# Performance work log

Measured on AMD Instinct MI355X. Metric: run time of the kernel, lower is better.

The kernel has to match this reference:

```python
import jax, jax.numpy as jnp
import numpy as np

N_HEAD = 16
D_MODEL = 1024
D_HEAD = D_MODEL // N_HEAD
B, T = 2, 2048


def setup_inputs() -> dict:
    key = jax.random.key(0)
    k1, k2, k3 = jax.random.split(key, 3)
    x = jax.random.normal(k1, (B, T, D_MODEL), dtype=jnp.float32)
    w_attn = jax.random.normal(k2, (3 * D_MODEL, D_MODEL), dtype=jnp.float32) * (D_MODEL ** -0.5)
    w_proj = jax.random.normal(k3, (D_MODEL, D_MODEL), dtype=jnp.float32) * (D_MODEL ** -0.5)
    return {"x": x, "w_attn": w_attn, "w_proj": w_proj}


def _rms_norm(x):
    eps = jnp.asarray(jnp.finfo(x.dtype).eps, x.dtype)
    var = jnp.mean(jnp.square(x), axis=-1, keepdims=True)
    return x * jax.lax.rsqrt(var + eps)


def _rotate_half(x):
    x1, x2 = jnp.split(x, 2, axis=-1)
    return jnp.concatenate((-x2, x1), axis=-1)


def reference(x, w_attn, w_proj):
    Bx, Tx, C = x.shape
    qkv = jnp.einsum('btc,fc->btf', x, w_attn)  # [B,T,3C]
    q, k, v = jnp.split(qkv, 3, axis=-1)
    # [B, H, T, Dh]
    q = q.reshape(Bx, Tx, N_HEAD, D_HEAD).transpose(0, 2, 1, 3)
    k = k.reshape(Bx, Tx, N_HEAD, D_HEAD).transpose(0, 2, 1, 3)
    v = v.reshape(Bx, Tx, N_HEAD, D_HEAD).transpose(0, 2, 1, 3)
    # QK RMSNorm (no learned weight)
    q = _rms_norm(q)
    k = _rms_norm(k)
    # Rotary embedding over full d_head: freqs tiled twice
    inv_freq = 1.0 / (10000.0 ** (jnp.arange(0, D_HEAD, 2, dtype=jnp.float32) / D_HEAD))
    t = jnp.arange(Tx, dtype=jnp.float32)
    freqs = jnp.einsum('i,j->ij', t, inv_freq)  # [T, Dh/2]
    emb = jnp.concatenate((freqs, freqs), axis=-1)  # [T, Dh]
    cos = jnp.cos(emb)[None, None, :, :]
    sin = jnp.sin(emb)[None, None, :, :]
    q = q * cos + _rotate_half(q) * sin
    k = k * cos + _rotate_half(k) * sin
    # Causal SDPA
    scale = D_HEAD ** -0.5
    scores = jnp.einsum('bhqd,bhkd->bhqk', q, k) * scale
    causal = jnp.tril(jnp.ones((Tx, Tx), dtype=bool))
    scores = jnp.where(causal[None, None], scores, jnp.asarray(-jnp.inf, scores.dtype))
    attn = jax.nn.softmax(scores, axis=-1)
    y = jnp.einsum('bhqk,bhkd->bhqd', attn, v)
    y = y.transpose(0, 2, 1, 3).reshape(Bx, Tx, C)
    return jnp.einsum('btc,oc->bto', y, w_proj)
```

## Files before the change

kernel.cpp:

```cpp
#include <hip/hip_runtime.h>
#include <cstdint>
#include <cstddef>


typedef short bf16x8 __attribute__((ext_vector_type(8)));
typedef float floatx4 __attribute__((ext_vector_type(4)));
typedef float floatx2 __attribute__((ext_vector_type(2)));
typedef unsigned short ushortx8 __attribute__((ext_vector_type(8)));
typedef unsigned short ushortx4 __attribute__((ext_vector_type(4)));
typedef unsigned int uintx2 __attribute__((ext_vector_type(2)));

#define DEVI __device__ __forceinline__

DEVI float bf2f(unsigned short u) {
    unsigned int x = ((unsigned int)u) << 16;
    return __builtin_bit_cast(float, x);
}
DEVI unsigned short f2bf(float f) {
    unsigned int u = __builtin_bit_cast(unsigned int, f);
    u += 0x7fffu + ((u >> 16) & 1u);
    return (unsigned short)(u >> 16);
}
DEVI unsigned int pkbf2(float a, float b) {
    unsigned int ua = __builtin_bit_cast(unsigned int, a) + 0x8000u;
    unsigned int ub = __builtin_bit_cast(unsigned int, b) + 0x8000u;
    return __builtin_amdgcn_perm(ub, ua, 0x07060302);
}

DEVI void glds16(const unsigned short* g, unsigned short* l) {
    __builtin_amdgcn_global_load_lds(
        (const __attribute__((address_space(1))) unsigned int*)g,
        (__attribute__((address_space(3))) unsigned int*)l, 16, 0, 0);
}

DEVI void cast8(unsigned short* dst, const float* src) {
    floatx4 a = *(const floatx4*)src;
    floatx4 b = *(const floatx4*)(src + 4);
    ushortx8 o;
    o[0] = f2bf(a[0]); o[1] = f2bf(a[1]); o[2] = f2bf(a[2]); o[3] = f2bf(a[3]);
    o[4] = f2bf(b[0]); o[5] = f2bf(b[1]); o[6] = f2bf(b[2]); o[7] = f2bf(b[3]);
    *(ushortx8*)dst = o;
}

__global__ __launch_bounds__(256)
void cast_inputs(const float* __restrict__ x, const float* __restrict__ wa,
                 const float* __restrict__ wp,
                 unsigned short* __restrict__ xb, unsigned short* __restrict__ wab,
                 unsigned short* __restrict__ wpb, float* __restrict__ ropetab)
{
    size_t g = (size_t)blockIdx.x * 256 + threadIdx.x;
    size_t stride = (size_t)gridDim.x * 256;
    for (size_t i = g; i < (4194304 / 8); i += stride) cast8(xb  + i * 8, x  + i * 8);
    for (size_t i = g; i < (3145728 / 8); i += stride) cast8(wab + i * 8, wa + i * 8);
    for (size_t i = g; i < (1048576 / 8); i += stride) cast8(wpb + i * 8, wp + i * 8);
    for (size_t i = g; i < 65536; i += stride) {
        int t = (int)(i >> 5), f = (int)(i & 31);
        float ang = (float)t * __expf(-(float)f * 0.28782313662425572f);
        float sn, cs;
        __sincosf(ang, &sn, &cs);
        ropetab[2 * i]     = cs;
        ropetab[2 * i + 1] = sn;
    }
}

__global__ __launch_bounds__(512, 2)
void gemm_qkv_8ph(const unsigned short* __restrict__ A,
                  const unsigned short* __restrict__ B,
                  const float* __restrict__ ropetab,
                  unsigned short* __restrict__ Cqk,
                  unsigned short* __restrict__ Vt)
{
    __shared__ __align__(16) unsigned short lds[2][2][256 * 64];

    const int tid  = threadIdx.x;
    const int lane = tid & 63;
    const int w    = tid >> 6;
    const int wm   = w >> 2;
    const int wn   = w & 3;
    const int quad = lane >> 4;
    const int lm   = lane & 15;

    const int lin = blockIdx.y * 12 + blockIdx.x;
    const int s   = (lin & 7) * 24 + (lin >> 3);
    const int m0  = (s / 12) * 256;
    const int n0  = (s % 12) * 256;

    const int srow = tid >> 3;
    const int scol = (((tid & 7) ^ ((tid >> 3) & 7)) * 8);
    const int ldst = w * 512;

#define STG_A(u, WBi, kq) glds16(&A[(size_t)(m0 + (u) * 64 + srow) * 1024 + (kq) + scol], \
                                 &lds[WBi][0][(u) * 4096 + ldst])
#define STG_B(u, WBi, kq) glds16(&B[(size_t)(n0 + (u) * 64 + srow) * 1024 + (kq) + scol], \
                                 &lds[WBi][1][(u) * 4096 + ldst])
#define RD_A(RBi, rrow, kk) (*(const bf16x8*)&lds[RBi][0][(rrow) * 64 + ((((kk) * 4 + quad) ^ ((rrow) & 7)) * 8)])
#define RD_B(RBi, rrow, kk) (*(const bf16x8*)&lds[RBi][1][(rrow) * 64 + ((((kk) * 4 + quad) ^ ((rrow) & 7)) * 8)])

    floatx4 acc[8][4] = {};
    bf16x8 afr[4][2];
    bf16x8 bfr[4][2];

#define MQ(MB, JB)                                                              \
  do {                                                                          \
    _Pragma("unroll")                                                           \
    for (int kk = 0; kk < 2; ++kk)                                              \
      _Pragma("unroll")                                                         \
      for (int mi = 0; mi < 4; ++mi)                                            \
        _Pragma("unroll")                                                       \
        for (int j2 = 0; j2 < 2; ++j2)                                          \
          acc[(MB) + mi][(JB) + j2] = __builtin_amdgcn_mfma_f32_16x16x32_bf16(  \
              afr[mi][kk], bfr[(JB) + j2][kk], acc[(MB) + mi][(JB) + j2], 0, 0, 0); \
  } while (0)

#define TILE(RBi, WBi, KT, LASTF)                                               \
  do {                                                                          \
    const int kn = ((KT) + 1) * 64;                                             \
    if (!(LASTF)) { STG_B(0, WBi, kn); STG_B(1, WBi, kn); }                     \
    _Pragma("unroll")                                                           \
    for (int kk = 0; kk < 2; ++kk) {                                            \
      _Pragma("unroll")                                                         \
      for (int mi = 0; mi < 4; ++mi)                                            \
        afr[mi][kk] = RD_A(RBi, wm * 128 + mi * 16 + lm, kk);                   \
      _Pragma("unroll")                                                         \
      for (int j2 = 0; j2 < 2; ++j2)                                            \
        bfr[j2][kk] = RD_B(RBi, wn * 64 + j2 * 16 + lm, kk);                    \
    }                                                                           \
    asm volatile("s_waitcnt lgkmcnt(8)" ::: "memory");                          \
    __builtin_amdgcn_s_barrier();                                               \
    asm volatile("s_waitcnt lgkmcnt(0)" ::: "memory");                          \
    __builtin_amdgcn_s_setprio(1); MQ(0, 0); __builtin_amdgcn_s_setprio(0);     \
    __builtin_amdgcn_s_barrier();                                               \
    if (!(LASTF)) { STG_B(2, WBi, kn); STG_B(3, WBi, kn); }                     \
    _Pragma("unroll")                                                           \
    for (int kk = 0; kk < 2; ++kk)                                              \
      _Pragma("unroll")                                                         \
      for (int j2 = 0; j2 < 2; ++j2)                                            \
        bfr[2 + j2][kk] = RD_B(RBi, wn * 64 + (2 + j2) * 16 + lm, kk);          \
    if (!(LASTF)) { asm volatile("s_waitcnt vmcnt(4)" ::: "memory"); }          \
    else          { asm volatile("s_waitcnt vmcnt(0)" ::: "memory"); }          \
    __builtin_amdgcn_s_barrier();                                               \
    asm volatile("s_waitcnt lgkmcnt(0)" ::: "memory");                          \
    __builtin_amdgcn_s_setprio(1); MQ(0, 2); __builtin_amdgcn_s_setprio(0);     \
    __builtin_amdgcn_s_barrier();                                               \
    if (!(LASTF)) { STG_A(0, WBi, kn); STG_A(2, WBi, kn); }                     \
    _Pragma("unroll")                                                           \
    for (int kk = 0; kk < 2; ++kk)                                              \
      _Pragma("unroll")                                                         \
      for (int mi = 0; mi < 4; ++mi)                                            \
        afr[mi][kk] = RD_A(RBi, wm * 128 + 64 + mi * 16 + lm, kk);              \
    __builtin_amdgcn_s_barrier();                                               \
    asm volatile("s_waitcnt lgkmcnt(0)" ::: "memory");                          \
    __builtin_amdgcn_s_setprio(1); MQ(4, 2); __builtin_amdgcn_s_setprio(0);     \
    __builtin_amdgcn_s_barrier();                                               \
    if (!(LASTF)) { STG_A(1, WBi, kn); STG_A(3, WBi, kn);                       \
                    asm volatile("s_waitcnt vmcnt(2)" ::: "memory"); }          \
    __builtin_amdgcn_s_barrier();                                               \
    __builtin_amdgcn_s_setprio(1); MQ(4, 0); __builtin_amdgcn_s_setprio(0);     \
    __builtin_amdgcn_s_barrier();                                               \
  } while (0)

    STG_B(0, 0, 0); STG_B(1, 0, 0); STG_B(2, 0, 0); STG_B(3, 0, 0);
    STG_A(0, 0, 0); STG_A(2, 0, 0); STG_A(1, 0, 0); STG_A(3, 0, 0);
    asm volatile("s_waitcnt vmcnt(2)" ::: "memory");
    __builtin_amdgcn_s_barrier();

    for (int kt = 0; kt < 14; kt += 2) {
        TILE(0, 1, kt, false);
        TILE(1, 0, kt + 1, false);
    }
    TILE(0, 1, 14, false);
    TILE(1, 0, 15, true);

    const bool is_v = (n0 + wn * 64) >= 2048;
    if (!is_v) {
        const floatx2* rtab = (const floatx2*)ropetab;
        #pragma unroll
        for (int mi = 0; mi < 8; ++mi) {
            float rn[4];
            #pragma unroll
            for (int r = 0; r < 4; ++r) {
                float ss = 0.0f;
                #pragma unroll
                for (int j = 0; j < 4; ++j) ss += acc[mi][j][r] * acc[mi][j][r];
                ss += __shfl_xor(ss, 1, 64);
                ss += __shfl_xor(ss, 2, 64);
                ss += __shfl_xor(ss, 4, 64);
                ss += __shfl_xor(ss, 8, 64);
                rn[r] = rsqrtf(ss * (1.0f / 64.0f) + 1.1920929e-07f);
            }
            #pragma unroll
            for (int r = 0; r < 4; ++r) {
                int row = m0 + wm * 128 + mi * 16 + quad * 4 + r;
                int t = row & 2047;
                floatx2 cs0 = rtab[t * 32 + lm];
                floatx2 cs1 = rtab[t * 32 + 16 + lm];
                float g = rn[r];
                #pragma unroll
                for (int j = 0; j < 4; ++j) {
                    int d = j * 16 + lm;
                    float cs = (j & 1) ? cs1[0] : cs0[0];
                    float sn = (j & 1) ? cs1[1] : cs0[1];
                    float v  = acc[mi][j][r] * g;
                    float vp = acc[mi][j ^ 2][r] * g;
                    float sgn = (d < 32) ? -1.0f : 1.0f;
                    Cqk[(size_t)row * 2048 + (n0 + wn * 64 + d)] =
                        f2bf(v * cs + sgn * vp * sn);
                }
            }
        }
    } else {
        #pragma unroll
        for (int mi = 0; mi < 8; ++mi)
            #pragma unroll
            for (int j = 0; j < 4; ++j) {
                int col  = n0 + wn * 64 + j * 16 + lm;
                int row0 = m0 + wm * 128 + mi * 16 + quad * 4;
                int bq = row0 >> 11, t0 = row0 & 2047;
                ushortx4 pk;
                #pragma unroll
                for (int r = 0; r < 4; ++r) pk[r] = f2bf(acc[mi][j][r]);
                *(ushortx4*)&Vt[((size_t)(bq * 1024 + (col - 2048))) * 2048 + t0] = pk;
            }
    }
#undef TILE
#undef MQ
#undef RD_A
#undef RD_B
#undef STG_A
#undef STG_B
}

template <int BN, int BK>
__global__ __launch_bounds__(256)
void gemm_bt(const unsigned short* __restrict__ A, const unsigned short* __restrict__ B,
             float* __restrict__ Cf, int M, int N, int K)
{
    constexpr int WCOLS = (BN == 128) ? 2 : 1;
    constexpr int WROWS = 4 / WCOLS;
    constexpr int MI    = 128 / (16 * WROWS);
    constexpr int LPR   = BK / 8;
    constexpr int RPI   = 64 / LPR;

    __shared__ __align__(16) unsigned short As[128 * BK];
    __shared__ __align__(16) unsigned short Bs[BN * BK];

    const int tid  = threadIdx.x;
    const int lane = tid & 63;
    const int w    = tid >> 6;
    const int wm   = w / WCOLS, wn = w % WCOLS;
    const int quad = lane >> 4;
    const int lm   = lane & 15;
    const int m0 = blockIdx.y * 128;
    const int n0 = blockIdx.x * BN;
    const int sr = lane / LPR;
    const int sc = (lane % LPR) * 8;

    floatx4 acc[MI][4] = {};

    for (int k0 = 0; k0 < K; k0 += BK) {
        __syncthreads();
        #pragma unroll
        for (int i = 0; i < 32 / RPI; ++i) {
            int r = w * 32 + i * RPI;
            glds16(&A[(size_t)(m0 + r + sr) * K + k0 + sc], &As[r * BK]);
        }
        #pragma unroll
        for (int i = 0; i < (BN / 4) / RPI; ++i) {
            int r = w * (BN / 4) + i * RPI;
            glds16(&B[(size_t)(n0 + r + sr) * K + k0 + sc], &Bs[r * BK]);
        }
        __syncthreads();

        #pragma unroll
        for (int kk = 0; kk < BK / 32; ++kk) {
            bf16x8 a[MI];
            #pragma unroll
            for (int i = 0; i < MI; ++i)
                a[i] = *(const bf16x8*)&As[(wm * (16 * MI) + i * 16 + lm) * BK + kk * 32 + quad * 8];
            #pragma unroll
            for (int j = 0; j < 4; ++j) {
                bf16x8 b = *(const bf16x8*)&Bs[(wn * 64 + j * 16 + lm) * BK + kk * 32 + quad * 8];
                #pragma unroll
                for (int i = 0; i < MI; ++i)
                    acc[i][j] = __builtin_amdgcn_mfma_f32_16x16x32_bf16(a[i], b, acc[i][j], 0, 0, 0);
            }
        }
    }

    #pragma unroll
    for (int i = 0; i < MI; ++i)
        #pragma unroll
        for (int j = 0; j < 4; ++j) {
            int col  = n0 + wn * 64 + j * 16 + lm;
            int row0 = m0 + wm * (16 * MI) + i * 16 + quad * 4;
            #pragma unroll
            for (int r = 0; r < 4; ++r)
                Cf[(size_t)(row0 + r) * N + col] = acc[i][j][r];
        }
}

#define ATTN_STEP(KSc, VSc, KSn, VSn, KT, DG, LAST)                            \
  do {                                                                         \
    if (!(LAST)) {                                                             \
      *(ushortx8*)&(KSn)[r0 * LD + pc] = kreg;                                 \
      *(ushortx8*)&(VSn)[r0 * LD + pc] = vreg;                                 \
      if ((KT) + 2 <= lastk) {                                                 \
        kreg = *(const ushortx8*)kp0; vreg = *(const ushortx8*)vp0;            \
        kp0 += (size_t)64 * 2048; vp0 += 64;                                   \
      }                                                                        \
    }                                                                          \
    floatx4 sa[4] = {};                                                        \
    _Pragma("unroll")                                                          \
    for (int kk = 0; kk < 2; ++kk)                                             \
      _Pragma("unroll")                                                        \
      for (int j = 0; j < 4; ++j) {                                            \
        bf16x8 kf = *(const bf16x8*)&(KSc)[(j * 16 + lm) * LD + kk * 32 + quad * 8]; \
        sa[j] = __builtin_amdgcn_mfma_f32_16x16x32_bf16(kf, qf[kk], sa[j], 0, 0, 0); \
      }                                                                        \
    _Pragma("unroll")                                                          \
    for (int j = 0; j < 4; ++j) {                                              \
      float p0 = exp2f(sa[j][0] * c1 - c2);                                    \
      float p1 = exp2f(sa[j][1] * c1 - c2);                                    \
      float p2 = exp2f(sa[j][2] * c1 - c2);                                    \
      float p3 = exp2f(sa[j][3] * c1 - c2);                                    \
      if (DG) {                                                                \
        int kb = (KT) * 64 + j * 16 + quad * 4;                                \
        if (kb + 0 > qrow) p0 = 0.0f;                                          \
        if (kb + 1 > qrow) p1 = 0.0f;                                          \
        if (kb + 2 > qrow) p2 = 0.0f;                                          \
        if (kb + 3 > qrow) p3 = 0.0f;                                          \
      }                                                                        \
      uintx2 pk;                                                               \
      pk[0] = pkbf2(p0, p1);                                                   \
      pk[1] = pkbf2(p2, p3);                                                   \
      *(uintx2*)&QPs[(w * 16 + lm) * LD + j * 16 + quad * 4] = pk;             \
    }                                                                          \
    _Pragma("unroll")                                                          \
    for (int kk = 0; kk < 2; ++kk) {                                           \
      bf16x8 pf = *(const bf16x8*)&QPs[(w * 16 + lm) * LD + kk * 32 + quad * 8]; \
      _Pragma("unroll")                                                        \
      for (int j = 0; j < 4; ++j) {                                            \
        bf16x8 vf = *(const bf16x8*)&(VSc)[(j * 16 + lm) * LD + kk * 32 + quad * 8]; \
        o[j] = __builtin_amdgcn_mfma_f32_16x16x32_bf16(pf, vf, o[j], 0, 0, 0); \
      }                                                                        \
      l_acc = __builtin_amdgcn_mfma_f32_16x16x32_bf16(pf, ones, l_acc, 0, 0, 0); \
    }                                                                          \
    if (!(LAST)) __syncthreads();                                              \
  } while (0)

__global__ __launch_bounds__(512)
void attention(const unsigned short* __restrict__ qk,
               const unsigned short* __restrict__ Vt,
               unsigned short* __restrict__ Y)
{
    constexpr int LD = 72;
    __shared__ __align__(16) unsigned short QPs[128 * LD];
    __shared__ __align__(16) unsigned short Ks0[64 * LD];
    __shared__ __align__(16) unsigned short Ks1[64 * LD];
    __shared__ __align__(16) unsigned short Vs0[64 * LD];
    __shared__ __align__(16) unsigned short Vs1[64 * LD];

    const int tid  = threadIdx.x;
    const int lane = tid & 63;
    const int w    = tid >> 6;
    const int quad = lane >> 4;
    const int lm   = lane & 15;

    const int bh = blockIdx.x;
    const int qt = 15 - blockIdx.y;
    const int b  = bh >> 4, h = bh & 15;
    const int q0 = qt * 128;
    const int qrow = q0 + w * 16 + lm;
    const int lastk = 2 * qt + 1;

    const int r0 = tid >> 3, pc = (tid & 7) * 8;
    const unsigned short* kp0 = qk + (size_t)b * 2048 * 2048 + 1024 + h * 64
                              + (size_t)r0 * 2048 + pc;
    const unsigned short* vp0 = Vt + (size_t)bh * 64 * 2048 + (size_t)r0 * 2048 + pc;

    #pragma unroll
    for (int i = 0; i < 2; ++i) {
        int c = i * 512 + tid, row = c >> 3, col = (c & 7) * 8;
        *(ushortx8*)&QPs[row * LD + col] =
            *(const ushortx8*)&qk[((size_t)(b * 2048 + q0 + row)) * 2048 + h * 64 + col];
    }

    ushortx8 kreg = *(const ushortx8*)kp0;
    ushortx8 vreg = *(const ushortx8*)vp0;
    kp0 += (size_t)64 * 2048; vp0 += 64;
    *(ushortx8*)&Ks0[r0 * LD + pc] = kreg;
    *(ushortx8*)&Vs0[r0 * LD + pc] = vreg;
    if (lastk >= 1) {
        kreg = *(const ushortx8*)kp0; vreg = *(const ushortx8*)vp0;
        kp0 += (size_t)64 * 2048; vp0 += 64;
    }
    __syncthreads();

    bf16x8 qf[2];
    #pragma unroll
    for (int kk = 0; kk < 2; ++kk)
        qf[kk] = *(const bf16x8*)&QPs[(w * 16 + lm) * LD + kk * 32 + quad * 8];

    bf16x8 ones;
    #pragma unroll
    for (int i = 0; i < 8; ++i) ones[i] = (short)0x3F80;

    floatx4 o[4] = {};
    floatx4 l_acc = {};
    const float c1 = 0.125f * 1.44269504f;
    const float c2 = 8.0f   * 1.44269504f;

    int kt = 0;
    for (; kt + 3 < 2 * qt + 2; kt += 2) {
        ATTN_STEP(Ks0, Vs0, Ks1, Vs1, kt,     false, false);
        ATTN_STEP(Ks1, Vs1, Ks0, Vs0, kt + 1, false, false);
    }
    ATTN_STEP(Ks0, Vs0, Ks1, Vs1, kt,     true, false);
    ATTN_STEP(Ks1, Vs1, Ks0, Vs0, kt + 1, true, true);

    float rinv[4];
    #pragma unroll
    for (int r = 0; r < 4; ++r) rinv[r] = 1.0f / l_acc[r];

    #pragma unroll
    for (int j = 0; j < 4; ++j) {
        int colg = h * 64 + j * 16 + lm;
        #pragma unroll
        for (int r = 0; r < 4; ++r) {
            int rowg = q0 + w * 16 + quad * 4 + r;
            Y[((size_t)(b * 2048 + rowg)) * 1024 + colg] = f2bf(o[j][r] * rinv[r]);
        }
    }
}

extern "C" void kernel_launch(void* const* d_in, const int* in_sizes, int n_in,
                              void* d_out, int out_size, void* d_ws, size_t ws_size,
                              hipStream_t stream)
{
    const float* x      = (const float*)d_in[0];
    const float* w_attn = (const float*)d_in[1];
    const float* w_proj = (const float*)d_in[2];
    float* out = (float*)d_out;

    unsigned short* qkbuf = (unsigned short*)d_ws;
    unsigned short* Vtb   = qkbuf + (size_t)4096 * 2048;
    unsigned short* y     = Vtb   + (size_t)32 * 64 * 2048;
    unsigned short* wpb   = y     + (size_t)4096 * 1024;
    unsigned short* xb  = (unsigned short*)d_out;
    unsigned short* wab = xb + (size_t)4096 * 1024;
    float* ropetab = (float*)(wab + (size_t)3072 * 1024);

    dim3 blk(256);
    cast_inputs<<<dim3(1024), blk, 0, stream>>>(x, w_attn, w_proj, xb, wab, wpb, ropetab);
    gemm_qkv_8ph<<<dim3(12, 16), dim3(512), 0, stream>>>(xb, wab, ropetab, qkbuf, Vtb);
    attention<<<dim3(32, 16), dim3(512), 0, stream>>>(qkbuf, Vtb, y);
    gemm_bt<64, 64>
        <<<dim3(16, 32), blk, 0, stream>>>(y, wpb, out, 4096, 1024, 1024);
}
```

Before: 178.7 us.

## Give each attention wave two query row tiles and XOR-swizzle shared memory

The attention kernel now runs 256 threads per block (4 waves), and each wave handles 32 query rows instead of 16. Each K and V fragment read from shared memory therefore feeds two MFMAs, which halves LDS reads per unit of work. The padded LD=72 layout is replaced with an unpadded 64-wide layout that uses XOR swizzling to avoid bank conflicts, which also shrinks the shared-memory footprint. The cost is more accumulator registers per thread and fewer waves per block to hide latency, with launch bounds set to 3 blocks per CU.

```diff
diff --git a/kernel.cpp b/kernel.cpp
--- a/kernel.cpp
+++ b/kernel.cpp
@@ -299,114 +299,135 @@
         }
 }
 
+#define ATTN_EXP(SA, QROW, PROW, KT, DG)                                       \
+  do {                                                                         \
+    _Pragma("unroll")                                                          \
+    for (int j = 0; j < 4; ++j) {                                              \
+      float p0 = exp2f((SA)[j][0] * c1 - c2);                                  \
+      float p1 = exp2f((SA)[j][1] * c1 - c2);                                  \
+      float p2 = exp2f((SA)[j][2] * c1 - c2);                                  \
+      float p3 = exp2f((SA)[j][3] * c1 - c2);                                  \
+      if (DG) {                                                                \
+        int kb = (KT) * 64 + j * 16 + quad * 4;                                \
+        if (kb + 0 > (QROW)) p0 = 0.0f;                                        \
+        if (kb + 1 > (QROW)) p1 = 0.0f;                                        \
+        if (kb + 2 > (QROW)) p2 = 0.0f;                                        \
+        if (kb + 3 > (QROW)) p3 = 0.0f;                                        \
+      }                                                                        \
+      uintx2 pk;                                                               \
+      pk[0] = pkbf2(p0, p1);                                                   \
+      pk[1] = pkbf2(p2, p3);                                                   \
+      *(uintx2*)&QPs[(PROW) * 64 + (((2 * j + (quad >> 1)) ^ sx) * 8) + (quad & 1) * 4] = pk; \
+    }                                                                          \
+  } while (0)
+
 #define ATTN_STEP(KSc, VSc, KSn, VSn, KT, DG, LAST)                            \
   do {                                                                         \
     if (!(LAST)) {                                                             \
-      *(ushortx8*)&(KSn)[r0 * LD + pc] = kreg;                                 \
-      *(ushortx8*)&(VSn)[r0 * LD + pc] = vreg;                                 \
+      *(ushortx8*)&(KSn)[wkA] = kregA; *(ushortx8*)&(KSn)[wkB] = kregB;        \
+      *(ushortx8*)&(VSn)[wkA] = vregA; *(ushortx8*)&(VSn)[wkB] = vregB;        \
       if ((KT) + 2 <= lastk) {                                                 \
-        kreg = *(const ushortx8*)kp0; vreg = *(const ushortx8*)vp0;            \
-        kp0 += (size_t)64 * 2048; vp0 += 64;                                   \
+        kregA = *(const ushortx8*)kpA; kregB = *(const ushortx8*)kpB;          \
+        vregA = *(const ushortx8*)vpA; vregB = *(const ushortx8*)vpB;          \
+        kpA += (size_t)64 * 2048; kpB += (size_t)64 * 2048;                    \
+        vpA += 64; vpB += 64;                                                  \
       }                                                                        \
     }                                                                          \
-    floatx4 sa[4] = {};                                                        \
+    floatx4 sa0[4] = {}, sa1[4] = {};                                          \
     _Pragma("unroll")                                                          \
     for (int kk = 0; kk < 2; ++kk)                                             \
       _Pragma("unroll")                                                        \
       for (int j = 0; j < 4; ++j) {                                            \
-        bf16x8 kf = *(const bf16x8*)&(KSc)[(j * 16 + lm) * LD + kk * 32 + quad * 8]; \
-        sa[j] = __builtin_amdgcn_mfma_f32_16x16x32_bf16(kf, qf[kk], sa[j], 0, 0, 0); \
+        bf16x8 kf = *(const bf16x8*)&(KSc)[(j * 16 + lm) * 64 + (((kk * 4 + quad) ^ sx) * 8)]; \
+        sa0[j] = __builtin_amdgcn_mfma_f32_16x16x32_bf16(kf, qf0[kk], sa0[j], 0, 0, 0); \
+        sa1[j] = __builtin_amdgcn_mfma_f32_16x16x32_bf16(kf, qf1[kk], sa1[j], 0, 0, 0); \
       }                                                                        \
-    _Pragma("unroll")                                                          \
-    for (int j = 0; j < 4; ++j) {                                              \
-      float p0 = exp2f(sa[j][0] * c1 - c2);                                    \
-      float p1 = exp2f(sa[j][1] * c1 - c2);                                    \
-      float p2 = exp2f(sa[j][2] * c1 - c2);                                    \
-      float p3 = exp2f(sa[j][3] * c1 - c2);                                    \
-      if (DG) {                                                                \
-        int kb = (KT) * 64 + j * 16 + quad * 4;                                \
-        if (kb + 0 > qrow) p0 = 0.0f;                                          \
-        if (kb + 1 > qrow) p1 = 0.0f;                                          \
-        if (kb + 2 > qrow) p2 = 0.0f;                                          \
-        if (kb + 3 > qrow) p3 = 0.0f;                                          \
-      }                                                                        \
-      uintx2 pk;                                                               \
-      pk[0] = pkbf2(p0, p1);                                                   \
-      pk[1] = pkbf2(p2, p3);                                                   \
-      *(uintx2*)&QPs[(w * 16 + lm) * LD + j * 16 + quad * 4] = pk;             \
-    }                                                                          \
+    ATTN_EXP(sa0, qrow0, w * 32 + lm,      KT, DG);                            \
+    ATTN_EXP(sa1, qrow1, w * 32 + 16 + lm, KT, DG);                            \
     _Pragma("unroll")                                                          \
     for (int kk = 0; kk < 2; ++kk) {                                           \
-      bf16x8 pf = *(const bf16x8*)&QPs[(w * 16 + lm) * LD + kk * 32 + quad * 8]; \
+      bf16x8 pf0 = *(const bf16x8*)&QPs[(w * 32 + lm) * 64 + (((kk * 4 + quad) ^ sx) * 8)]; \
+      bf16x8 pf1 = *(const bf16x8*)&QPs[(w * 32 + 16 + lm) * 64 + (((kk * 4 + quad) ^ sx) * 8)]; \
       _Pragma("unroll")                                                        \
       for (int j = 0; j < 4; ++j) {                                            \
-        bf16x8 vf = *(const bf16x8*)&(VSc)[(j * 16 + lm) * LD + kk * 32 + quad * 8]; \
-        o[j] = __builtin_amdgcn_mfma_f32_16x16x32_bf16(pf, vf, o[j], 0, 0, 0); \
+        bf16x8 vf = *(const bf16x8*)&(VSc)[(j * 16 + lm) * 64 + (((kk * 4 + quad) ^ sx) * 8)]; \
+        o0[j] = __builtin_amdgcn_mfma_f32_16x16x32_bf16(pf0, vf, o0[j], 0, 0, 0); \
+        o1[j] = __builtin_amdgcn_mfma_f32_16x16x32_bf16(pf1, vf, o1[j], 0, 0, 0); \
       }                                                                        \
-      l_acc = __builtin_amdgcn_mfma_f32_16x16x32_bf16(pf, ones, l_acc, 0, 0, 0); \
+      l0 = __builtin_amdgcn_mfma_f32_16x16x32_bf16(pf0, ones, l0, 0, 0, 0);    \
+      l1 = __builtin_amdgcn_mfma_f32_16x16x32_bf16(pf1, ones, l1, 0, 0, 0);    \
     }                                                                          \
     if (!(LAST)) __syncthreads();                                              \
   } while (0)
 
-__global__ __launch_bounds__(512)
+__global__ __launch_bounds__(256, 3)
 void attention(const unsigned short* __restrict__ qk,
                const unsigned short* __restrict__ Vt,
                unsigned short* __restrict__ Y)
 {
-    constexpr int LD = 72;
-    __shared__ __align__(16) unsigned short QPs[128 * LD];
-    __shared__ __align__(16) unsigned short Ks0[64 * LD];
-    __shared__ __align__(16) unsigned short Ks1[64 * LD];
-    __shared__ __align__(16) unsigned short Vs0[64 * LD];
-    __shared__ __align__(16) unsigned short Vs1[64 * LD];
+    __shared__ __align__(16) unsigned short QPs[128 * 64];
+    __shared__ __align__(16) unsigned short Ks0[64 * 64];
+    __shared__ __align__(16) unsigned short Ks1[64 * 64];
+    __shared__ __align__(16) unsigned short Vs0[64 * 64];
+    __shared__ __align__(16) unsigned short Vs1[64 * 64];
 
     const int tid  = threadIdx.x;
     const int lane = tid & 63;
     const int w    = tid >> 6;
     const int quad = lane >> 4;
     const int lm   = lane & 15;
+    const int sx   = lm & 7;
 
     const int bh = blockIdx.x;
     const int qt = 15 - blockIdx.y;
     const int b  = bh >> 4, h = bh & 15;
     const int q0 = qt * 128;
-    const int qrow = q0 + w * 16 + lm;
+    const int qrow0 = q0 + w * 32 + lm;
+    const int qrow1 = qrow0 + 16;
     const int lastk = 2 * qt + 1;
 
-    const int r0 = tid >> 3, pc = (tid & 7) * 8;
-    const unsigned short* kp0 = qk + (size_t)b * 2048 * 2048 + 1024 + h * 64
-                              + (size_t)r0 * 2048 + pc;
-    const unsigned short* vp0 = Vt + (size_t)bh * 64 * 2048 + (size_t)r0 * 2048 + pc;
-
-    #pragma unroll
-    for (int i = 0; i < 2; ++i) {
-        int c = i * 512 + tid, row = c >> 3, col = (c & 7) * 8;
-        *(ushortx8*)&QPs[row * LD + col] =
-            *(const ushortx8*)&qk[((size_t)(b * 2048 + q0 + row)) * 2048 + h * 64 + col];
-    }
-
-    ushortx8 kreg = *(const ushortx8*)kp0;
-    ushortx8 vreg = *(const ushortx8*)vp0;
-    kp0 += (size_t)64 * 2048; vp0 += 64;
-    *(ushortx8*)&Ks0[r0 * LD + pc] = kreg;
-    *(ushortx8*)&Vs0[r0 * LD + pc] = vreg;
-    if (lastk >= 1) {
-        kreg = *(const ushortx8*)kp0; vreg = *(const ushortx8*)vp0;
-        kp0 += (size_t)64 * 2048; vp0 += 64;
-    }
+    const int sr  = tid >> 3;
+    const int sch = tid & 7;
+    const int swz = ((sch ^ (sr & 7)) * 8);
+    const int wkA = sr * 64 + swz;
+    const int wkB = (sr + 32) * 64 + swz;
+
+    const unsigned short* kpA = qk + (size_t)b * 2048 * 2048 + 1024 + h * 64
+                              + (size_t)sr * 2048 + sch * 8;
+    const unsigned short* kpB = kpA + (size_t)32 * 2048;
+    const unsigned short* vpA = Vt + (size_t)bh * 64 * 2048 + (size_t)sr * 2048 + sch * 8;
+    const unsigned short* vpB = vpA + (size_t)32 * 2048;
+
+    #pragma unroll
+    for (int p = 0; p < 4; ++p) {
+        int row = p * 32 + sr;
+        *(ushortx8*)&QPs[row * 64 + swz] =
+            *(const ushortx8*)&qk[((size_t)(b * 2048 + q0 + row)) * 2048 + h * 64 + sch * 8];
+    }
+
+    ushortx8 kregA = *(const ushortx8*)kpA, kregB = *(const ushortx8*)kpB;
+    ushortx8 vregA = *(const ushortx8*)vpA, vregB = *(const ushortx8*)vpB;
+    kpA += (size_t)64 * 2048; kpB += (size_t)64 * 2048; vpA += 64; vpB += 64;
+    *(ushortx8*)&Ks0[wkA] = kregA; *(ushortx8*)&Ks0[wkB] = kregB;
+    *(ushortx8*)&Vs0[wkA] = vregA; *(ushortx8*)&Vs0[wkB] = vregB;
+    kregA = *(const ushortx8*)kpA; kregB = *(const ushortx8*)kpB;
+    vregA = *(const ushortx8*)vpA; vregB = *(const ushortx8*)vpB;
+    kpA += (size_t)64 * 2048; kpB += (size_t)64 * 2048; vpA += 64; vpB += 64;
     __syncthreads();
 
-    bf16x8 qf[2];
-    #pragma unroll
-    for (int kk = 0; kk < 2; ++kk)
-        qf[kk] = *(const bf16x8*)&QPs[(w * 16 + lm) * LD + kk * 32 + quad * 8];
+    bf16x8 qf0[2], qf1[2];
+    #pragma unroll
+    for (int kk = 0; kk < 2; ++kk) {
+        qf0[kk] = *(const bf16x8*)&QPs[(w * 32 + lm) * 64 + (((kk * 4 + quad) ^ sx) * 8)];
+        qf1[kk] = *(const bf16x8*)&QPs[(w * 32 + 16 + lm) * 64 + (((kk * 4 + quad) ^ sx) * 8)];
+    }
 
     bf16x8 ones;
     #pragma unroll
     for (int i = 0; i < 8; ++i) ones[i] = (short)0x3F80;
 
-    floatx4 o[4] = {};
-    floatx4 l_acc = {};
+    floatx4 o0[4] = {}, o1[4] = {};
+    floatx4 l0 = {}, l1 = {};
     const float c1 = 0.125f * 1.44269504f;
     const float c2 = 8.0f   * 1.44269504f;
 
@@ -418,17 +439,18 @@
     ATTN_STEP(Ks0, Vs0, Ks1, Vs1, kt,     true, false);
     ATTN_STEP(Ks1, Vs1, Ks0, Vs0, kt + 1, true, true);
 
-    float rinv[4];
-    #pragma unroll
-    for (int r = 0; r < 4; ++r) rinv[r] = 1.0f / l_acc[r];
+    float rinv0[4], rinv1[4];
+    #pragma unroll
+    for (int r = 0; r < 4; ++r) { rinv0[r] = 1.0f / l0[r]; rinv1[r] = 1.0f / l1[r]; }
 
     #pragma unroll
     for (int j = 0; j < 4; ++j) {
         int colg = h * 64 + j * 16 + lm;
         #pragma unroll
         for (int r = 0; r < 4; ++r) {
-            int rowg = q0 + w * 16 + quad * 4 + r;
-            Y[((size_t)(b * 2048 + rowg)) * 1024 + colg] = f2bf(o[j][r] * rinv[r]);
+            int rowg0 = q0 + w * 32 + quad * 4 + r;
+            Y[((size_t)(b * 2048 + rowg0)) * 1024 + colg] = f2bf(o0[j][r] * rinv0[r]);
+            Y[((size_t)(b * 2048 + rowg0 + 16)) * 1024 + colg] = f2bf(o1[j][r] * rinv1[r]);
         }
     }
 }
@@ -453,7 +475,7 @@
     dim3 blk(256);
     cast_inputs<<<dim3(1024), blk, 0, stream>>>(x, w_attn, w_proj, xb, wab, wpb, ropetab);
     gemm_qkv_8ph<<<dim3(12, 16), dim3(512), 0, stream>>>(xb, wab, ropetab, qkbuf, Vtb);
-    attention<<<dim3(32, 16), dim3(512), 0, stream>>>(qkbuf, Vtb, y);
+    attention<<<dim3(32, 16), dim3(256), 0, stream>>>(qkbuf, Vtb, y);
     gemm_bt<64, 64>
         <<<dim3(16, 32), blk, 0, stream>>>(y, wpb, out, 4096, 1024, 1024);
 }
```

New measurement: 185.8 us. +4.0%, slower.
